# Kernel optimization log

Hardware: AMD Instinct MI355X
Metric: run time of the kernel (lower is better)

The kernel has to match this reference:

```python
import math
import jax, jax.numpy as jnp
import numpy as np

NUM_HEADS = 12
HEAD_DIM = 64
HIDDEN = NUM_HEADS * HEAD_DIM  # 768
SEQ = 4096


def setup_inputs() -> dict:
    key = jax.random.key(0)
    ks = jax.random.split(key, 7)
    s = 0.02  # BERT-style init scale for weights
    return {
        "hidden_states": jax.random.normal(ks[0], (1, SEQ, HIDDEN), jnp.float32),
        "Wq": jax.random.normal(ks[1], (HIDDEN, HIDDEN), jnp.float32) * s,
        "bq": jax.random.normal(ks[2], (HIDDEN,), jnp.float32) * s,
        "Wk": jax.random.normal(ks[3], (HIDDEN, HIDDEN), jnp.float32) * s,
        "bk": jax.random.normal(ks[4], (HIDDEN,), jnp.float32) * s,
        "Wv": jax.random.normal(ks[5], (HIDDEN, HIDDEN), jnp.float32) * s,
        "bv": jax.random.normal(ks[6], (HIDDEN,), jnp.float32) * s,
    }


def _split_heads(z):
    # [S, HIDDEN] -> [H, S, dh]
    S = z.shape[0]
    return jnp.transpose(z.reshape(S, NUM_HEADS, HEAD_DIM), (1, 0, 2))


def reference(hidden_states, Wq, bq, Wk, bk, Wv, bv):
    # batch is squeezed in the original module (kernel is unbatched)
    x = hidden_states[0]  # [S, D]
    q = _split_heads(x @ Wq.T + bq)  # [H, S, dh]
    k = _split_heads(x @ Wk.T + bk)  # [H, S, dh]
    scale = 1.0 / math.sqrt(HEAD_DIM)
    scores = jnp.einsum('hqd,hkd->hqk', q, k) * scale  # [H, S, S]
    probs = jax.nn.softmax(scores, axis=-1)
    # multi_rand_attn_cuda approximates P @ (x @ Wv^T + bv) via CDF-driven
    # Monte-Carlo column sampling of Wv; its expectation is the exact product,
    # which is the correctness baseline computed here.
    v = _split_heads(x @ Wv.T + bv)  # [H, S, dh]
    ctx = jnp.einsum('hqk,hkd->hqd', probs, v)  # [H, S, dh]
    ctx = jnp.transpose(ctx, (1, 0, 2)).reshape(x.shape[0], HIDDEN)
    return ctx[None]  # [1, S, D]
```

## Files before the change

kernel.cpp:

```cpp
#include <hip/hip_runtime.h>
#include <stdint.h>


typedef float    f32x4 __attribute__((ext_vector_type(4)));
typedef _Float16 h16x8 __attribute__((ext_vector_type(8)));
typedef _Float16 h16x4 __attribute__((ext_vector_type(4)));
typedef _Float16 h16x2 __attribute__((ext_vector_type(2)));
typedef __fp16   fp16x2 __attribute__((ext_vector_type(2)));
typedef unsigned short u16;

#define MFMA32(A, B, C) __builtin_amdgcn_mfma_f32_16x16x32_f16((A), (B), (C), 0, 0, 0)
#define ZERO4 ((f32x4){0.f, 0.f, 0.f, 0.f})

#define SEQ 4096
#define HID 768
#define NH  12
#define DH  64

#define CEXP 0.18033688011112042f

#define WAITV(N) asm volatile("s_waitcnt vmcnt(" #N ")" ::: "memory")
#define SBAR()   __builtin_amdgcn_s_barrier()
#define SCHED0() __builtin_amdgcn_sched_barrier(0)

__device__ __forceinline__ u16 f2h(float f) {
  union { _Float16 h; u16 u; } v;
  v.h = (_Float16)f;
  return v.u;
}
__device__ __forceinline__ float h2f(u16 u) {
  union { u16 u; _Float16 h; } v;
  v.u = u;
  return (float)v.h;
}

__device__ __forceinline__ void gload_lds16(const void* g, void* l) {
  __builtin_amdgcn_global_load_lds(
      (__attribute__((address_space(1))) void*)(g),
      (__attribute__((address_space(3))) void*)(l),
      16, 0, 0);
}

__global__ __launch_bounds__(256) void cast_all_k(
    const float* __restrict__ x,  const float* __restrict__ wq,
    const float* __restrict__ wk, const float* __restrict__ wv,
    u16* __restrict__ xh,  u16* __restrict__ wqh,
    u16* __restrict__ wkh, u16* __restrict__ wvh)
{
  int i = blockIdx.x * 256 + threadIdx.x;
  const int NX4 = (SEQ * HID) / 4;
  const int NW4 = (HID * HID) / 4;
  const float4* src; ushort4* dst; int idx;
  if (i < NX4) {
    src = (const float4*)x; dst = (ushort4*)xh; idx = i;
  } else {
    int j = i - NX4;
    int w = j / NW4;
    idx = j - w * NW4;
    src = (const float4*)(w == 0 ? wq : (w == 1 ? wk : wv));
    dst = (ushort4*)(w == 0 ? wqh : (w == 1 ? wkh : wvh));
  }
  float4 v = src[idx];
  ushort4 o;
  o.x = f2h(v.x); o.y = f2h(v.y); o.z = f2h(v.z); o.w = f2h(v.w);
  dst[idx] = o;
}

__global__ __launch_bounds__(256, 3) void qkv_gemm_k(
    const u16* __restrict__ xh,
    const u16* __restrict__ wqh, const u16* __restrict__ wkh, const u16* __restrict__ wvh,
    const float* __restrict__ bq, const float* __restrict__ bk, const float* __restrict__ bv,
    u16* __restrict__ Qh, u16* __restrict__ Kh, u16* __restrict__ Vt)
{
  __shared__ u16 S[128 * 128];

  const int t = threadIdx.x;
  const int wave = t >> 6, lane = t & 63;
  const int m = lane & 15, quad = lane >> 4;

  const int lin = blockIdx.x + 6 * (blockIdx.y + 32 * blockIdx.z);
  const int o   = (lin & 7) * 72 + (lin >> 3);
  const int bz  = o / 192;
  const int rem = o - bz * 192;
  const int by  = rem / 6;
  const int bx  = rem - by * 6;
  const int z  = bz;
  const int n0 = bx * 128;
  const int m0 = by * 128;

  const u16*   W    = (z == 0) ? wqh : (z == 1) ? wkh : wvh;
  const float* bias = (z == 0) ? bq  : (z == 1) ? bk  : bv;

  const int wm = (wave >> 1) * 64;
  const int wn = (wave & 1) * 64;

  f32x4 acc[4][4];
#pragma unroll
  for (int i = 0; i < 4; i++)
#pragma unroll
    for (int j = 0; j < 4; j++) acc[i][j] = ZERO4;

  const int srow = wave * 8 + (lane >> 3);
  const int scg  = (lane & 7) ^ (srow & 7);
  const u16* gA = xh + (m0 + srow) * HID + scg * 8;
  const u16* gB = W  + (n0 + srow) * HID + scg * 8;
  u16* lA = S + wave * 512;
  u16* lB = S + 8192 + wave * 512;

  for (int k0 = 0; k0 < HID; k0 += 64) {
    __syncthreads();
#pragma unroll
    for (int c = 0; c < 4; c++) {
      gload_lds16(gA + c * 32 * HID + k0, lA + c * 2048);
      gload_lds16(gB + c * 32 * HID + k0, lB + c * 2048);
    }
    __syncthreads();

#pragma unroll
    for (int s = 0; s < 2; s++) {
      h16x8 af[4], bf[4];
#pragma unroll
      for (int i = 0; i < 4; i++)
        af[i] = *(const h16x8*)(S + (wm + i * 16 + m) * 64
                                + ((s * 4 + quad) ^ (m & 7)) * 8);
#pragma unroll
      for (int j = 0; j < 4; j++)
        bf[j] = *(const h16x8*)(S + 8192 + (wn + j * 16 + m) * 64
                                + ((s * 4 + quad) ^ (m & 7)) * 8);
#pragma unroll
      for (int i = 0; i < 4; i++)
#pragma unroll
        for (int j = 0; j < 4; j++)
          acc[i][j] = MFMA32(af[i], bf[j], acc[i][j]);
    }
  }

  __syncthreads();

  if (z < 2) {
    const float sc = (z == 0) ? CEXP : 1.0f;
#pragma unroll
    for (int i = 0; i < 4; i++) {
      int sl = wm + i * 16 + quad * 4;
#pragma unroll
      for (int j = 0; j < 4; j++) {
        int colp = wn + j * 16 + m;
        float bb = bias[n0 + colp];
        int c = colp >> 3, sub = colp & 7;
#pragma unroll
        for (int r = 0; r < 4; r++)
          S[(sl + r) * 128 + ((c ^ ((sl + r) & 15)) * 8) + sub] =
              f2h((acc[i][j][r] + bb) * sc);
      }
    }
    __syncthreads();
    u16* outp = (z == 0) ? Qh : Kh;
    const int ch = t & 15;
#pragma unroll
    for (int rr = 0; rr < 8; rr++) {
      int s = rr * 16 + (t >> 4);
      h16x8 v = *(const h16x8*)(S + s * 128 + ((ch ^ (s & 15)) * 8));
      *(h16x8*)(outp + (m0 + s) * HID + n0 + ch * 8) = v;
    }
  } else {
#pragma unroll
    for (int i = 0; i < 4; i++) {
      int sl = wm + i * 16 + quad * 4;
      int vp = (sl & ~31) + ((sl >> 2) & 3) * 8 + ((sl >> 4) & 1) * 4;
#pragma unroll
      for (int j = 0; j < 4; j++) {
        int nl = wn + j * 16 + m;
        float bb = bias[n0 + nl];
        h16x4 o4;
        o4[0] = (_Float16)(acc[i][j][0] + bb);
        o4[1] = (_Float16)(acc[i][j][1] + bb);
        o4[2] = (_Float16)(acc[i][j][2] + bb);
        o4[3] = (_Float16)(acc[i][j][3] + bb);
        *(h16x4*)(S + nl * 128 + (((vp >> 3) ^ (nl & 15)) * 8) + (vp & 7)) = o4;
      }
    }
    __syncthreads();
    const int ch = t & 15;
#pragma unroll
    for (int rr = 0; rr < 8; rr++) {
      int n = rr * 16 + (t >> 4);
      h16x8 v = *(const h16x8*)(S + n * 128 + ((ch ^ (n & 15)) * 8));
      *(h16x8*)(Vt + (n0 + n) * SEQ + m0 + ch * 8) = v;
    }
  }
}


__device__ __forceinline__ void stage_kv(const u16* gKb, const u16* gVb,
                                         u16* lK, u16* lV, int kv0)
{
#pragma unroll
  for (int c = 0; c < 2; c++) {
    gload_lds16(gKb + (kv0 + c * 32) * HID, lK + c * 2048);
    gload_lds16(gVb + c * 32 * SEQ + kv0,   lV + c * 2048);
  }
}

__device__ __forceinline__ void attn_compute(
    const u16* __restrict__ Kb, const u16* __restrict__ Vb,
    const h16x8 (&qf)[2][2], f32x4 (&O)[2][4], f32x4 (&Lacc)[2],
    h16x8 onesv, int m, int quad)
{
#pragma unroll
  for (int p = 0; p < 2; ++p) {
    const int krow0 = 32 * p + m;
    const int krow1 = krow0 + 16;
    h16x8 kb00 = *(const h16x8*)(Kb + krow0 * 64 + ((    quad) ^ (m & 7)) * 8);
    h16x8 kb01 = *(const h16x8*)(Kb + krow0 * 64 + ((4 + quad) ^ (m & 7)) * 8);
    h16x8 kb10 = *(const h16x8*)(Kb + krow1 * 64 + ((    quad) ^ (m & 7)) * 8);
    h16x8 kb11 = *(const h16x8*)(Kb + krow1 * 64 + ((4 + quad) ^ (m & 7)) * 8);

    h16x8 vb[4];
#pragma unroll
    for (int jd = 0; jd < 4; jd++) {
      int d = jd * 16 + m;
      vb[jd] = *(const h16x8*)(Vb + d * 64 + (((p * 4 + quad) ^ (m & 7)) * 8));
    }

#pragma unroll
    for (int qn = 0; qn < 2; qn++) {
      __builtin_amdgcn_s_setprio(1);
      f32x4 S0 = MFMA32(kb00, qf[qn][0], ZERO4);
      S0       = MFMA32(kb01, qf[qn][1], S0);
      f32x4 S1 = MFMA32(kb10, qf[qn][0], ZERO4);
      S1       = MFMA32(kb11, qf[qn][1], S1);
      __builtin_amdgcn_s_setprio(0);

      float e0 = __builtin_amdgcn_exp2f(S0[0]);
      float e1 = __builtin_amdgcn_exp2f(S0[1]);
      float e2 = __builtin_amdgcn_exp2f(S0[2]);
      float e3 = __builtin_amdgcn_exp2f(S0[3]);
      float e4 = __builtin_amdgcn_exp2f(S1[0]);
      float e5 = __builtin_amdgcn_exp2f(S1[1]);
      float e6 = __builtin_amdgcn_exp2f(S1[2]);
      float e7 = __builtin_amdgcn_exp2f(S1[3]);

      fp16x2 p01 = __builtin_amdgcn_cvt_pkrtz(e0, e1);
      fp16x2 p23 = __builtin_amdgcn_cvt_pkrtz(e2, e3);
      fp16x2 p45 = __builtin_amdgcn_cvt_pkrtz(e4, e5);
      fp16x2 p67 = __builtin_amdgcn_cvt_pkrtz(e6, e7);
      h16x2 q01 = __builtin_bit_cast(h16x2, p01);
      h16x2 q23 = __builtin_bit_cast(h16x2, p23);
      h16x2 q45 = __builtin_bit_cast(h16x2, p45);
      h16x2 q67 = __builtin_bit_cast(h16x2, p67);
      h16x4 pl = __builtin_shufflevector(q01, q23, 0, 1, 2, 3);
      h16x4 ph = __builtin_shufflevector(q45, q67, 0, 1, 2, 3);
      h16x8 pa = __builtin_shufflevector(pl, ph, 0, 1, 2, 3, 4, 5, 6, 7);

      __builtin_amdgcn_s_setprio(1);
#pragma unroll
      for (int jd = 0; jd < 4; jd++)
        O[qn][jd] = MFMA32(pa, vb[jd], O[qn][jd]);
      Lacc[qn] = MFMA32(pa, onesv, Lacc[qn]);
      __builtin_amdgcn_s_setprio(0);
    }
  }
}

__global__ __launch_bounds__(256, 3) void attn_k(
    const u16* __restrict__ Qh, const u16* __restrict__ Kh, const u16* __restrict__ Vt,
    float* __restrict__ out0, u16* __restrict__ Op1, float* __restrict__ Lp)
{
  __shared__ u16 Ks[3][64 * 64];
  __shared__ u16 Vs[3][64 * 64];

  const int t = threadIdx.x;
  const int wave = t >> 6, lane = t & 63;
  const int m = lane & 15, quad = lane >> 4;

  const int lin = blockIdx.x + 32 * (blockIdx.y + 12 * blockIdx.z);
  const int swz = (lin & 7) * 96 + (lin >> 3);
  const int h  = (swz >> 5) % 12;
  const int q0 = (swz & 31) * 128;
  const int sp = swz / 384;
  const int kvbase = sp * 2048;

  h16x8 qf[2][2];
#pragma unroll
  for (int qn = 0; qn < 2; qn++)
#pragma unroll
    for (int ks = 0; ks < 2; ks++)
      qf[qn][ks] = *(const h16x8*)(Qh + (q0 + wave * 32 + qn * 16 + m) * HID
                                   + h * DH + ks * 32 + quad * 8);

  f32x4 O[2][4];
#pragma unroll
  for (int qn = 0; qn < 2; qn++)
#pragma unroll
    for (int jd = 0; jd < 4; jd++) O[qn][jd] = ZERO4;
  f32x4 Lacc[2] = {ZERO4, ZERO4};

  h16x8 onesv;
#pragma unroll
  for (int j = 0; j < 8; j++) onesv[j] = (_Float16)1.0f;

  const int srow = wave * 8 + (lane >> 3);
  const int swzl = ((lane & 7) ^ (srow & 7)) * 8;
  const u16* gKb = Kh + srow * HID + h * DH + swzl;
  const u16* gVb = Vt + (h * DH + srow) * SEQ + swzl;
  u16* lK0 = &Ks[0][wave * 512]; u16* lV0 = &Vs[0][wave * 512];
  u16* lK1 = &Ks[1][wave * 512]; u16* lV1 = &Vs[1][wave * 512];
  u16* lK2 = &Ks[2][wave * 512]; u16* lV2 = &Vs[2][wave * 512];

  stage_kv(gKb, gVb, lK0, lV0, kvbase);
  stage_kv(gKb, gVb, lK1, lV1, kvbase + 64);

  for (int it = 0; it < 30; it += 3) {
    WAITV(4); SBAR(); SCHED0();
    stage_kv(gKb, gVb, lK2, lV2, kvbase + (it + 2) * 64);
    attn_compute(&Ks[0][0], &Vs[0][0], qf, O, Lacc, onesv, m, quad);
    SCHED0();

    WAITV(4); SBAR(); SCHED0();
    stage_kv(gKb, gVb, lK0, lV0, kvbase + (it + 3) * 64);
    attn_compute(&Ks[1][0], &Vs[1][0], qf, O, Lacc, onesv, m, quad);
    SCHED0();

    WAITV(4); SBAR(); SCHED0();
    stage_kv(gKb, gVb, lK1, lV1, kvbase + (it + 4) * 64);
    attn_compute(&Ks[2][0], &Vs[2][0], qf, O, Lacc, onesv, m, quad);
    SCHED0();
  }
  WAITV(4); SBAR(); SCHED0();
  attn_compute(&Ks[0][0], &Vs[0][0], qf, O, Lacc, onesv, m, quad);
  SCHED0();
  WAITV(0); SBAR(); SCHED0();
  attn_compute(&Ks[1][0], &Vs[1][0], qf, O, Lacc, onesv, m, quad);

#pragma unroll
  for (int qn = 0; qn < 2; qn++) {
    if (m == 0) {
#pragma unroll
      for (int r = 0; r < 4; r++)
        Lp[sp * NH * SEQ + h * SEQ + q0 + wave * 32 + qn * 16 + quad * 4 + r] =
            Lacc[qn][r];
    }
#pragma unroll
    for (int jd = 0; jd < 4; jd++) {
      int col = h * DH + jd * 16 + m;
#pragma unroll
      for (int r = 0; r < 4; r++) {
        int row = q0 + wave * 32 + qn * 16 + quad * 4 + r;
        if (sp == 0) out0[row * HID + col] = O[qn][jd][r];
        else         Op1[row * HID + col] = f2h(O[qn][jd][r]);
      }
    }
  }
}

__global__ __launch_bounds__(256) void reduce_k(
    float* __restrict__ out, const u16* __restrict__ Op1,
    const float* __restrict__ Lp)
{
  int i = blockIdx.x * 256 + threadIdx.x;
  int s  = i / 192;
  int c4 = i - s * 192;
  int h  = c4 >> 4;
  float L = Lp[h * SEQ + s] + Lp[NH * SEQ + h * SEQ + s];
  float inv = __builtin_amdgcn_rcpf(L);
  float4 a = ((const float4*)out)[i];
  ushort4 b = ((const ushort4*)Op1)[i];
  float4 r;
  r.x = (a.x + h2f(b.x)) * inv;
  r.y = (a.y + h2f(b.y)) * inv;
  r.z = (a.z + h2f(b.z)) * inv;
  r.w = (a.w + h2f(b.w)) * inv;
  ((float4*)out)[i] = r;
}

extern "C" void kernel_launch(void* const* d_in, const int* in_sizes, int n_in,
                              void* d_out, int out_size, void* d_ws, size_t ws_size,
                              hipStream_t stream) {
  const float* x  = (const float*)d_in[0];
  const float* Wq = (const float*)d_in[1];
  const float* bq = (const float*)d_in[2];
  const float* Wk = (const float*)d_in[3];
  const float* bk = (const float*)d_in[4];
  const float* Wv = (const float*)d_in[5];
  const float* bv = (const float*)d_in[6];
  float* out = (float*)d_out;

  char* ws = (char*)d_ws;
  u16* Qh  = (u16*)(ws);
  u16* Kh  = (u16*)(ws + 6291456);
  u16* Vt  = (u16*)(ws + 12582912);
  u16* xh  = (u16*)(ws + 18874368);
  u16* wqh = (u16*)(ws + 25165824);
  u16* wkh = (u16*)(ws + 26345472);
  u16* wvh = (u16*)(ws + 27525120);
  u16*   Op1 = (u16*)(ws + 18874368);
  float* Lp  = (float*)(ws + 25165824);

  cast_all_k<<<4800, 256, 0, stream>>>(x, Wq, Wk, Wv, xh, wqh, wkh, wvh);
  qkv_gemm_k<<<dim3(6, 32, 3), 256, 0, stream>>>(xh, wqh, wkh, wvh,
                                                 bq, bk, bv, Qh, Kh, Vt);
  attn_k<<<dim3(32, NH, 2), 256, 0, stream>>>(Qh, Kh, Vt, out, Op1, Lp);
  reduce_k<<<3072, 256, 0, stream>>>(out, Op1, Lp);
}
```

Baseline: 158.0 us.

## Double-buffer LDS in QKV GEMM to overlap global loads with MFMA

```diff
diff --git a/kernel.cpp b/kernel.cpp
--- a/kernel.cpp
+++ b/kernel.cpp
@@ -66,13 +66,39 @@
   dst[idx] = o;
 }
 
-__global__ __launch_bounds__(256, 3) void qkv_gemm_k(
+
+__device__ __forceinline__ void qcompute64(const u16* buf, f32x4 (&acc)[4][4],
+                                           int wm, int wn, int m, int quad)
+{
+#pragma unroll
+  for (int s = 0; s < 2; s++) {
+    h16x8 af[4], bf[4];
+#pragma unroll
+    for (int i = 0; i < 4; i++)
+      af[i] = *(const h16x8*)(buf + (wm + i * 16 + m) * 64
+                              + ((s * 4 + quad) ^ (m & 7)) * 8);
+#pragma unroll
+    for (int j = 0; j < 4; j++)
+      bf[j] = *(const h16x8*)(buf + 8192 + (wn + j * 16 + m) * 64
+                              + ((s * 4 + quad) ^ (m & 7)) * 8);
+    __builtin_amdgcn_s_setprio(1);
+#pragma unroll
+    for (int i = 0; i < 4; i++)
+#pragma unroll
+      for (int j = 0; j < 4; j++)
+        acc[i][j] = MFMA32(af[i], bf[j], acc[i][j]);
+    __builtin_amdgcn_s_setprio(0);
+  }
+}
+
+__global__ __launch_bounds__(256, 2) void qkv_gemm_k(
     const u16* __restrict__ xh,
     const u16* __restrict__ wqh, const u16* __restrict__ wkh, const u16* __restrict__ wvh,
     const float* __restrict__ bq, const float* __restrict__ bk, const float* __restrict__ bv,
     u16* __restrict__ Qh, u16* __restrict__ Kh, u16* __restrict__ Vt)
 {
-  __shared__ u16 S[128 * 128];
+  __shared__ u16 S[2][16384];
+  u16* Sf = &S[0][0];
 
   const int t = threadIdx.x;
   const int wave = t >> 6, lane = t & 63;
@@ -104,35 +130,31 @@
   const int scg  = (lane & 7) ^ (srow & 7);
   const u16* gA = xh + (m0 + srow) * HID + scg * 8;
   const u16* gB = W  + (n0 + srow) * HID + scg * 8;
-  u16* lA = S + wave * 512;
-  u16* lB = S + 8192 + wave * 512;
-
-  for (int k0 = 0; k0 < HID; k0 += 64) {
-    __syncthreads();
-#pragma unroll
-    for (int c = 0; c < 4; c++) {
-      gload_lds16(gA + c * 32 * HID + k0, lA + c * 2048);
-      gload_lds16(gB + c * 32 * HID + k0, lB + c * 2048);
-    }
-    __syncthreads();
-
-#pragma unroll
-    for (int s = 0; s < 2; s++) {
-      h16x8 af[4], bf[4];
-#pragma unroll
-      for (int i = 0; i < 4; i++)
-        af[i] = *(const h16x8*)(S + (wm + i * 16 + m) * 64
-                                + ((s * 4 + quad) ^ (m & 7)) * 8);
-#pragma unroll
-      for (int j = 0; j < 4; j++)
-        bf[j] = *(const h16x8*)(S + 8192 + (wn + j * 16 + m) * 64
-                                + ((s * 4 + quad) ^ (m & 7)) * 8);
-#pragma unroll
-      for (int i = 0; i < 4; i++)
-#pragma unroll
-        for (int j = 0; j < 4; j++)
-          acc[i][j] = MFMA32(af[i], bf[j], acc[i][j]);
-    }
+
+#define QSTAGE(b, k0)                                                     \
+  {                                                                       \
+    u16* lA = &S[b][0]    + wave * 512;                                   \
+    u16* lB = &S[b][8192] + wave * 512;                                   \
+    _Pragma("unroll")                                                     \
+    for (int c = 0; c < 4; c++) {                                         \
+      gload_lds16(gA + c * 32 * HID + (k0), lA + c * 2048);               \
+      gload_lds16(gB + c * 32 * HID + (k0), lB + c * 2048);               \
+    }                                                                     \
+  }
+
+  QSTAGE(0, 0)
+
+#pragma unroll
+  for (int kt = 0; kt < 12; kt += 2) {
+    WAITV(0); SBAR(); SCHED0();
+    if (kt + 1 < 12) QSTAGE(1, (kt + 1) * 64)
+    qcompute64(&S[0][0], acc, wm, wn, m, quad);
+    SCHED0();
+
+    WAITV(0); SBAR(); SCHED0();
+    if (kt + 2 < 12) QSTAGE(0, (kt + 2) * 64)
+    qcompute64(&S[1][0], acc, wm, wn, m, quad);
+    SCHED0();
   }
 
   __syncthreads();
@@ -149,7 +171,7 @@
         int c = colp >> 3, sub = colp & 7;
 #pragma unroll
         for (int r = 0; r < 4; r++)
-          S[(sl + r) * 128 + ((c ^ ((sl + r) & 15)) * 8) + sub] =
+          Sf[(sl + r) * 128 + ((c ^ ((sl + r) & 15)) * 8) + sub] =
               f2h((acc[i][j][r] + bb) * sc);
       }
     }
@@ -159,7 +181,7 @@
 #pragma unroll
     for (int rr = 0; rr < 8; rr++) {
       int s = rr * 16 + (t >> 4);
-      h16x8 v = *(const h16x8*)(S + s * 128 + ((ch ^ (s & 15)) * 8));
+      h16x8 v = *(const h16x8*)(Sf + s * 128 + ((ch ^ (s & 15)) * 8));
       *(h16x8*)(outp + (m0 + s) * HID + n0 + ch * 8) = v;
     }
   } else {
@@ -176,7 +198,7 @@
         o4[1] = (_Float16)(acc[i][j][1] + bb);
         o4[2] = (_Float16)(acc[i][j][2] + bb);
         o4[3] = (_Float16)(acc[i][j][3] + bb);
-        *(h16x4*)(S + nl * 128 + (((vp >> 3) ^ (nl & 15)) * 8) + (vp & 7)) = o4;
+        *(h16x4*)(Sf + nl * 128 + (((vp >> 3) ^ (nl & 15)) * 8) + (vp & 7)) = o4;
       }
     }
     __syncthreads();
@@ -184,7 +206,7 @@
 #pragma unroll
     for (int rr = 0; rr < 8; rr++) {
       int n = rr * 16 + (t >> 4);
-      h16x8 v = *(const h16x8*)(S + n * 128 + ((ch ^ (n & 15)) * 8));
+      h16x8 v = *(const h16x8*)(Sf + n * 128 + ((ch ^ (n & 15)) * 8));
       *(h16x8*)(Vt + (n0 + n) * SEQ + m0 + ch * 8) = v;
     }
   }
```

New measurement: 159.3 us. No clear change (+0.8%).

## Fuse split-KV reduction into attention via atomic last-block combine

Applied to the files above, without the earlier changes.

```diff
diff --git a/kernel.cpp b/kernel.cpp
--- a/kernel.cpp
+++ b/kernel.cpp
@@ -77,16 +77,9 @@
   const int t = threadIdx.x;
   const int wave = t >> 6, lane = t & 63;
   const int m = lane & 15, quad = lane >> 4;
-
-  const int lin = blockIdx.x + 6 * (blockIdx.y + 32 * blockIdx.z);
-  const int o   = (lin & 7) * 72 + (lin >> 3);
-  const int bz  = o / 192;
-  const int rem = o - bz * 192;
-  const int by  = rem / 6;
-  const int bx  = rem - by * 6;
-  const int z  = bz;
-  const int n0 = bx * 128;
-  const int m0 = by * 128;
+  const int z  = blockIdx.z;
+  const int n0 = blockIdx.x * 128;
+  const int m0 = blockIdx.y * 128;
 
   const u16*   W    = (z == 0) ? wqh : (z == 1) ? wkh : wvh;
   const float* bias = (z == 0) ? bq  : (z == 1) ? bk  : bv;
@@ -264,7 +257,8 @@
 
 __global__ __launch_bounds__(256, 3) void attn_k(
     const u16* __restrict__ Qh, const u16* __restrict__ Kh, const u16* __restrict__ Vt,
-    float* __restrict__ out0, u16* __restrict__ Op1, float* __restrict__ Lp)
+    float* __restrict__ out0, u16* __restrict__ Op1, float* __restrict__ Lp,
+    unsigned* __restrict__ flags)
 {
   __shared__ u16 Ks[3][64 * 64];
   __shared__ u16 Vs[3][64 * 64];
@@ -351,26 +345,36 @@
       }
     }
   }
-}
-
-__global__ __launch_bounds__(256) void reduce_k(
-    float* __restrict__ out, const u16* __restrict__ Op1,
-    const float* __restrict__ Lp)
-{
-  int i = blockIdx.x * 256 + threadIdx.x;
-  int s  = i / 192;
-  int c4 = i - s * 192;
-  int h  = c4 >> 4;
-  float L = Lp[h * SEQ + s] + Lp[NH * SEQ + h * SEQ + s];
-  float inv = __builtin_amdgcn_rcpf(L);
-  float4 a = ((const float4*)out)[i];
-  ushort4 b = ((const ushort4*)Op1)[i];
-  float4 r;
-  r.x = (a.x + h2f(b.x)) * inv;
-  r.y = (a.y + h2f(b.y)) * inv;
-  r.z = (a.z + h2f(b.z)) * inv;
-  r.w = (a.w + h2f(b.w)) * inv;
-  ((float4*)out)[i] = r;
+
+  __syncthreads();
+  unsigned* flagp = flags + (q0 >> 7) * NH + h;
+  volatile unsigned* lflag = (volatile unsigned*)&Ks[0][0];
+  if (t == 0) {
+    __threadfence();
+    *lflag = atomicAdd(flagp, 1u);
+  }
+  __syncthreads();
+  if (*lflag == 1u) {
+    __threadfence();
+    const float* LpA = Lp + h * SEQ;
+    const float* LpB = Lp + NH * SEQ + h * SEQ;
+#pragma unroll
+    for (int qn = 0; qn < 2; qn++) {
+#pragma unroll
+      for (int jd = 0; jd < 4; jd++) {
+        int col = h * DH + jd * 16 + m;
+#pragma unroll
+        for (int r = 0; r < 4; r++) {
+          int row = q0 + wave * 32 + qn * 16 + quad * 4 + r;
+          float inv = __builtin_amdgcn_rcpf(LpA[row] + LpB[row]);
+          float mine = O[qn][jd][r];
+          float other = (sp == 0) ? h2f(Op1[row * HID + col])
+                                  : out0[row * HID + col];
+          out0[row * HID + col] = (mine + other) * inv;
+        }
+      }
+    }
+  }
 }
 
 extern "C" void kernel_launch(void* const* d_in, const int* in_sizes, int n_in,
@@ -393,12 +397,13 @@
   u16* wqh = (u16*)(ws + 25165824);
   u16* wkh = (u16*)(ws + 26345472);
   u16* wvh = (u16*)(ws + 27525120);
-  u16*   Op1 = (u16*)(ws + 18874368);
-  float* Lp  = (float*)(ws + 25165824);
+  u16*      Op1   = (u16*)(ws + 18874368);
+  float*    Lp    = (float*)(ws + 25165824);
+  unsigned* flags = (unsigned*)(ws + 25559040);
 
   cast_all_k<<<4800, 256, 0, stream>>>(x, Wq, Wk, Wv, xh, wqh, wkh, wvh);
   qkv_gemm_k<<<dim3(6, 32, 3), 256, 0, stream>>>(xh, wqh, wkh, wvh,
                                                  bq, bk, bv, Qh, Kh, Vt);
-  attn_k<<<dim3(32, NH, 2), 256, 0, stream>>>(Qh, Kh, Vt, out, Op1, Lp);
-  reduce_k<<<3072, 256, 0, stream>>>(out, Op1, Lp);
-}
+  hipMemsetAsync(flags, 0, 384 * sizeof(unsigned), stream);
+  attn_k<<<dim3(32, NH, 2), 256, 0, stream>>>(Qh, Kh, Vt, out, Op1, Lp, flags);
+}
```

Result: slower. 288.1 us (+82.3%).
